# Kernel tuning notes

Measured on AMD Instinct MI355X. Metric: run time of the kernel, lower is better.

Reference implementation:

```python
import jax, jax.numpy as jnp
import numpy as np

B, T, D_IN, H, NUM_OUT = 64, 2048, 128, 512, 128


def _lstm_layer(x, W_ih, W_hh, b_ih, b_hh):
    # x: [B, T, D]; W_ih: [4H, D]; W_hh: [4H, H]; gate order i, f, g, o (PyTorch)
    Bsz = x.shape[0]
    Hh = W_hh.shape[1]
    # Precompute the input projection for all timesteps in one big GEMM: [B, T, 4H]
    xg = jnp.einsum('btd,gd->btg', x, W_ih) + b_ih + b_hh
    h0 = jnp.zeros((Bsz, Hh), x.dtype)
    c0 = jnp.zeros((Bsz, Hh), x.dtype)

    def step(carry, xg_t):
        h, c = carry
        gates = xg_t + h @ W_hh.T  # [B, 4H]
        i, f, g, o = jnp.split(gates, 4, axis=-1)
        i = jax.nn.sigmoid(i)
        f = jax.nn.sigmoid(f)
        g = jnp.tanh(g)
        o = jax.nn.sigmoid(o)
        c = f * c + i * g
        h = o * jnp.tanh(c)
        return (h, c), h

    (_, _), hs = jax.lax.scan(step, (h0, c0), jnp.swapaxes(xg, 0, 1))  # hs: [T, B, H]
    return jnp.swapaxes(hs, 0, 1)  # [B, T, H]


def setup_inputs() -> dict:
    key = jax.random.key(0)
    ks = jax.random.split(key, 7)

    def xavier(k, shape):
        fan_in, fan_out = shape[1], shape[0]
        lim = np.sqrt(6.0 / (fan_in + fan_out))
        return jax.random.uniform(k, shape, jnp.float32, -lim, lim)

    return {
        'x': jax.random.normal(ks[0], (B, T, D_IN), jnp.float32),
        'W_ih0': xavier(ks[1], (4 * H, D_IN)),
        'W_hh0': xavier(ks[2], (4 * H, H)),
        'b_ih0': jnp.zeros((4 * H,), jnp.float32),
        'b_hh0': jnp.zeros((4 * H,), jnp.float32),
        'W_ih1': xavier(ks[3], (4 * H, H)),
        'W_hh1': xavier(ks[4], (4 * H, H)),
        'b_ih1': jnp.zeros((4 * H,), jnp.float32),
        'b_hh1': jnp.zeros((4 * H,), jnp.float32),
        'fc_w': xavier(ks[5], (NUM_OUT, H)),
        'fc_b': jnp.zeros((NUM_OUT,), jnp.float32),
    }


def reference(x, W_ih0, W_hh0, b_ih0, b_hh0, W_ih1, W_hh1, b_ih1, b_hh1, fc_w, fc_b):
    out = _lstm_layer(x, W_ih0, W_hh0, b_ih0, b_hh0)
    out = _lstm_layer(out, W_ih1, W_hh1, b_ih1, b_hh1)
    # fc applied to last timestep only
    return out[:, -1, :] @ fc_w.T + fc_b
```

## Files before the change

kernel.cpp:

```cpp
#include <hip/hip_runtime.h>
#include <hip/hip_fp16.h>
#include <math.h>

#define BB    64
#define TT    2048
#define DIN   128
#define HH    512
#define NWG   256
#define NTHR  256
#define NUNITS 1152

typedef __attribute__((ext_vector_type(4))) unsigned int u32x4;
typedef __attribute__((ext_vector_type(8))) _Float16    f16x8;
typedef __attribute__((ext_vector_type(4))) float       f32x4;
typedef unsigned long long u64;

__device__ __forceinline__ float sigm(float v) { return 1.0f / (1.0f + expf(-v)); }

__device__ __forceinline__ u32x4 ld16m(const void* p) {
  u32x4 v;
  asm volatile("global_load_dwordx4 %0, %1, off sc0 sc1" : "=v"(v) : "v"(p) : "memory");
  return v;
}
__device__ __forceinline__ void st8m(void* p, u64 v) {
  __hip_atomic_store((u64*)p, v, __ATOMIC_RELAXED, __HIP_MEMORY_SCOPE_AGENT);
}
__device__ __forceinline__ u64 ld8m(const void* p) {
  return __hip_atomic_load((const u64*)p, __ATOMIC_RELAXED, __HIP_MEMORY_SCOPE_AGENT);
}

__global__ __launch_bounds__(64, 1) void prep_flush() {
  extern __shared__ char dummy[];
  if (threadIdx.x == 0) { __threadfence(); dummy[0] = 0; }
  __syncthreads();
}
__global__ void prep_zero(unsigned* w) {
  const int total = (4*BB*HH*2 + 8192) / 4;
  for (int i = blockIdx.x*blockDim.x + threadIdx.x; i < total; i += gridDim.x*blockDim.x)
    __hip_atomic_store(w + i, 0u, __ATOMIC_RELAXED, __HIP_MEMORY_SCOPE_AGENT);
}
__global__ void xcvt(const float* __restrict__ x, u64* __restrict__ xh) {
  const int N4 = BB*TT*DIN/4;
  const float4* x4 = reinterpret_cast<const float4*>(x);
  for (int i = blockIdx.x*blockDim.x + threadIdx.x; i < N4; i += gridDim.x*blockDim.x) {
    float4 v = x4[i];
    __half2 a = __floats2half2_rn(v.x, v.y);
    __half2 b = __floats2half2_rn(v.z, v.w);
    u64 u = ((u64)__builtin_bit_cast(unsigned, b) << 32) | (u64)__builtin_bit_cast(unsigned, a);
    __hip_atomic_store(&xh[i], u, __ATOMIC_RELAXED, __HIP_MEMORY_SCOPE_AGENT);
  }
}

__global__ __launch_bounds__(NTHR, 1) void lstm2_fb(
    const float* __restrict__ Wih0, const float* __restrict__ Whh0,
    const float* __restrict__ bih0, const float* __restrict__ bhh0,
    const float* __restrict__ Wih1, const float* __restrict__ Whh1,
    const float* __restrict__ bih1, const float* __restrict__ bhh1,
    const float* __restrict__ fcw,  const float* __restrict__ fcb,
    float* __restrict__ out, float* __restrict__ ws)
{
  extern __shared__ char smbase[];
  __half* hout = reinterpret_cast<__half*>(smbase + 18432);
  int*    dead = reinterpret_cast<int*>(smbase + 18944);

  const int tid  = threadIdx.x;
  const int wg   = blockIdx.x;
  const int lane = tid & 63;
  const int wv   = tid >> 6;

  const int grp  = wg >> 5;
  const int r    = wg & 31;
  const int bg8  = grp * 8;
  const int c0   = 16*r + 4*wv;

  __half* h0s = reinterpret_cast<__half*>(ws);
  __half* h1s = h0s + 2*BB*HH;
  unsigned* flg = reinterpret_cast<unsigned*>((char*)ws + 262144) + grp*32;
  const __half* xh = reinterpret_cast<const __half*>((char*)ws + 524288);

  const int rt   = lane & 15;
  const int gate = rt & 3;
  const int jc   = rt >> 2;
  const int kg   = lane >> 4;
  const int b15  = lane & 15;
  const int n0   = gate*HH + (c0 + jc);

  f16x8 af0[20];
#pragma unroll
  for (int m = 0; m < 20; ++m) {
    int k0 = 32*m + 8*kg;
    const float* srcp = (k0 < DIN) ? (Wih0 + (size_t)n0*DIN + k0)
                                   : (Whh0 + (size_t)n0*HH + (k0 - DIN));
    float4 a = *reinterpret_cast<const float4*>(srcp);
    float4 b = *reinterpret_cast<const float4*>(srcp + 4);
    f16x8 fr;
    fr[0]=(_Float16)a.x; fr[1]=(_Float16)a.y; fr[2]=(_Float16)a.z; fr[3]=(_Float16)a.w;
    fr[4]=(_Float16)b.x; fr[5]=(_Float16)b.y; fr[6]=(_Float16)b.z; fr[7]=(_Float16)b.w;
    af0[m] = fr;
  }
  f16x8 af1[32];
#pragma unroll
  for (int m = 0; m < 32; ++m) {
    int k0 = 32*m + 8*kg;
    const float* srcp = (k0 < HH) ? (Wih1 + (size_t)n0*HH + k0)
                                  : (Whh1 + (size_t)n0*HH + (k0 - HH));
    float4 a = *reinterpret_cast<const float4*>(srcp);
    float4 b = *reinterpret_cast<const float4*>(srcp + 4);
    f16x8 fr;
    fr[0]=(_Float16)a.x; fr[1]=(_Float16)a.y; fr[2]=(_Float16)a.z; fr[3]=(_Float16)a.w;
    fr[4]=(_Float16)b.x; fr[5]=(_Float16)b.y; fr[6]=(_Float16)b.z; fr[7]=(_Float16)b.w;
    af1[m] = fr;
  }

  const int cmy = c0 + kg;
  float bv0[4], bv1[4];
#pragma unroll
  for (int g = 0; g < 4; ++g) {
    bv0[g] = bih0[g*HH + cmy] + bhh0[g*HH + cmy];
    bv1[g] = bih1[g*HH + cmy] + bhh1[g*HH + cmy];
  }

  float cst0 = 0.f, cst1 = 0.f;
  const int beff = (b15 < 8) ? b15 : 7;
  const int bsw  = beff << 1;
  if (tid == 0) *dead = 0;
  __syncthreads();

  for (int st = 0; st <= TT; ++st) {
    const int tcur = (st < TT) ? st : (TT - 1);
    const __half* h0r = h0s + (size_t)(st & 1)*BB*HH;
    const __half* h1r = h1s + (size_t)(st & 1)*BB*HH;

    u32x4 stgL[5];
    int   physv[5];
#pragma unroll
    for (int ii = 0; ii < 5; ++ii) {
      int idx = tid + NTHR*ii;
      physv[ii] = -1;
      if (idx < NUNITS) {
        const __half* src; int phys;
        if (idx < 128)      { int b = idx>>4, u = idx&15;
          src = xh + (size_t)(bg8+b)*TT*DIN + (size_t)tcur*DIN + u*8;
          phys = b*16 + (u ^ ((b<<1)&15)); }
        else if (idx < 640) { int i2 = idx-128, b = i2>>6, u = i2&63;
          src = h0r + (size_t)(bg8+b)*HH + u*8;
          phys = 128 + b*64 + (u ^ (b<<1)); }
        else                { int i2 = idx-640, b = i2>>6, u = i2&63;
          src = h1r + (size_t)(bg8+b)*HH + u*8;
          phys = 640 + b*64 + (u ^ (b<<1)); }
        physv[ii] = phys;
        stgL[ii] = ld16m(src);
      }
    }
    asm volatile("s_waitcnt vmcnt(0)" ::: "memory");
    __builtin_amdgcn_sched_barrier(0);
#pragma unroll
    for (int ii = 0; ii < 5; ++ii)
      if (physv[ii] >= 0)
        *reinterpret_cast<u32x4*>(smbase + physv[ii]*16) = stgL[ii];
    __syncthreads();

    f32x4 a0a = {0.f,0.f,0.f,0.f}, a0b = a0a, a1a = a0a, a1b = a0a;
#pragma unroll
    for (int m = 0; m < 20; ++m) {
      int phys = (m < 4) ? (beff*16 + ((4*m + kg) ^ (bsw & 15)))
                         : (128 + beff*64 + ((4*(m-4) + kg) ^ bsw));
      f16x8 bf = *reinterpret_cast<const f16x8*>(smbase + phys*16);
      if (m & 1) a0b = __builtin_amdgcn_mfma_f32_16x16x32_f16(af0[m], bf, a0b, 0, 0, 0);
      else       a0a = __builtin_amdgcn_mfma_f32_16x16x32_f16(af0[m], bf, a0a, 0, 0, 0);
    }
#pragma unroll
    for (int m = 0; m < 32; ++m) {
      int phys = (m < 16) ? (128 + beff*64 + ((4*m + kg) ^ bsw))
                          : (640 + beff*64 + ((4*(m-16) + kg) ^ bsw));
      f16x8 bf = *reinterpret_cast<const f16x8*>(smbase + phys*16);
      if (m & 1) a1b = __builtin_amdgcn_mfma_f32_16x16x32_f16(af1[m], bf, a1b, 0, 0, 0);
      else       a1a = __builtin_amdgcn_mfma_f32_16x16x32_f16(af1[m], bf, a1a, 0, 0, 0);
    }
    f32x4 a0 = a0a + a0b;
    f32x4 a1 = a1a + a1b;

    if (st < TT) {
      float gi = sigm (a0[0] + bv0[0]);
      float gf = sigm (a0[1] + bv0[1]);
      float gg = tanhf(a0[2] + bv0[2]);
      float go = sigm (a0[3] + bv0[3]);
      cst0 = gf*cst0 + gi*gg;
      float hn = go * tanhf(cst0);
      if (b15 < 8) hout[(0*8 + b15)*16 + 4*wv + kg] = __float2half(hn);
    }
    if (st >= 1) {
      float gi = sigm (a1[0] + bv1[0]);
      float gf = sigm (a1[1] + bv1[1]);
      float gg = tanhf(a1[2] + bv1[2]);
      float go = sigm (a1[3] + bv1[3]);
      cst1 = gf*cst1 + gi*gg;
      float hn = go * tanhf(cst1);
      if (b15 < 8) hout[(1*8 + b15)*16 + 4*wv + kg] = __float2half(hn);
    }
    __syncthreads();

    if (tid < 64) {
      int layer = tid >> 5, q = tid & 31, b = q >> 2, part = q & 3;
      bool do_st = (layer == 0) ? (st < TT) : (st >= 1);
      if (do_st) {
        u64 v = *reinterpret_cast<u64*>(hout + (layer*8 + b)*16 + part*4);
        __half* base = (layer ? h1s : h0s) + (size_t)((st + 1) & 1)*BB*HH;
        st8m(base + (size_t)(bg8+b)*HH + 16*r + part*4, v);
      }
    }

    __syncthreads();
    if (wv == 0 && *dead == 0) {
      asm volatile("s_waitcnt vmcnt(0)" ::: "memory");
      if (lane == 0)
        __hip_atomic_store(flg + r, (unsigned)(st + 1),
                           __ATOMIC_RELAXED, __HIP_MEMORY_SCOPE_AGENT);
      long sp = 0;
      for (;;) {
        unsigned f = 0u;
        if (lane < 32)
          f = __hip_atomic_load(flg + lane, __ATOMIC_RELAXED, __HIP_MEMORY_SCOPE_AGENT);
        bool ok = (lane < 32) ? (f >= (unsigned)(st + 1)) : true;
        if (__all(ok)) break;
        __builtin_amdgcn_s_sleep(1);
        if (++sp > (1L << 22)) { if (lane == 0) *dead = 1; break; }
      }
      asm volatile("" ::: "memory");
    }
    __syncthreads();
  }

  {
    const __half* h1f = h1s + (size_t)BB*HH;
    int oi = tid >> 3, kp = tid & 7;
    int b  = oi >> 2, cc = oi & 3;
    int ocol = 4*r + cc;
    const u64* h8 = reinterpret_cast<const u64*>(h1f + (size_t)(bg8+b)*HH) + kp*16;
    const float* wrow = fcw + (size_t)ocol*HH + kp*64;
    float p = 0.f;
#pragma unroll
    for (int kk = 0; kk < 16; ++kk) {
      u64 v = ld8m(h8 + kk);
      __half2 hlo = __builtin_bit_cast(__half2, (unsigned)(v & 0xffffffffull));
      __half2 hhi = __builtin_bit_cast(__half2, (unsigned)(v >> 32));
      float2 flo = __half22float2(hlo), fhi = __half22float2(hhi);
      float4 w = *reinterpret_cast<const float4*>(wrow + kk*4);
      p += flo.x*w.x + flo.y*w.y + fhi.x*w.z + fhi.y*w.w;
    }
    p += __shfl_xor(p, 1);
    p += __shfl_xor(p, 2);
    p += __shfl_xor(p, 4);
    if (kp == 0) out[(size_t)(bg8+b)*128 + ocol] = p + fcb[ocol];
  }
}

__global__ void sentinel_fail(float* out, float v) { out[threadIdx.x] = v; }

extern "C" void kernel_launch(void* const* d_in, const int* in_sizes, int n_in,
                              void* d_out, int out_size, void* d_ws, size_t ws_size,
                              hipStream_t stream) {
  const float* x    = (const float*)d_in[0];
  const float* Wih0 = (const float*)d_in[1];
  const float* Whh0 = (const float*)d_in[2];
  const float* bih0 = (const float*)d_in[3];
  const float* bhh0 = (const float*)d_in[4];
  const float* Wih1 = (const float*)d_in[5];
  const float* Whh1 = (const float*)d_in[6];
  const float* bih1 = (const float*)d_in[7];
  const float* bhh1 = (const float*)d_in[8];
  const float* fcw  = (const float*)d_in[9];
  const float* fcb  = (const float*)d_in[10];
  float* out = (float*)d_out;
  float* ws  = (float*)d_ws;
  (void)in_sizes; (void)n_in; (void)out_size;

  const size_t need = 524288 + (size_t)BB*TT*DIN*2;
  if (ws_size < need) {
    sentinel_fail<<<1, 128, 0, stream>>>(out, 2.0e6f);
    return;
  }

  const int smem_bytes = 108*1024;
  hipFuncSetAttribute(reinterpret_cast<const void*>(&lstm2_fb),
                      hipFuncAttributeMaxDynamicSharedMemorySize, smem_bytes);
  hipFuncSetAttribute(reinterpret_cast<const void*>(&prep_flush),
                      hipFuncAttributeMaxDynamicSharedMemorySize, smem_bytes);

  (void)hipGetLastError();
  prep_flush<<<dim3(NWG), dim3(64), smem_bytes, stream>>>();
  xcvt<<<dim3(2048), dim3(NTHR), 0, stream>>>(
      x, reinterpret_cast<u64*>(reinterpret_cast<char*>(d_ws) + 524288));
  prep_zero<<<dim3(NWG), dim3(NTHR), 0, stream>>>((unsigned*)d_ws);
  lstm2_fb<<<dim3(NWG), dim3(NTHR), smem_bytes, stream>>>(
      Wih0, Whh0, bih0, bhh0, Wih1, Whh1, bih1, bhh1, fcw, fcb, out, ws);
  hipError_t e = hipGetLastError();
  if (e != hipSuccess) {
    sentinel_fail<<<1, 128, 0, stream>>>(out, 1.0e6f);
  }
}
```

Before: 8.455 ms.

## Split per-step grid barrier into two staggered flag phases per layer

Replaces the single end-of-step group barrier with two flag arrays. Layer-0 h is published and the layer-1 h buffer is read in a separate phase, and each workgroup polls only the flags it needs before loading. The layer-1 MFMA work on h0 now overlaps with waiting for other workgroups' h1 state. The intent is to shorten the serialized critical path of each timestep. It adds an extra __syncthreads and a second poll per step, and the double-buffer ordering becomes harder to verify.

```diff
diff --git a/kernel.cpp b/kernel.cpp
--- a/kernel.cpp
+++ b/kernel.cpp
@@ -8,7 +8,6 @@
 #define HH    512
 #define NWG   256
 #define NTHR  256
-#define NUNITS 1152
 
 typedef __attribute__((ext_vector_type(4))) unsigned int u32x4;
 typedef __attribute__((ext_vector_type(8))) _Float16    f16x8;
@@ -28,6 +27,20 @@
 __device__ __forceinline__ u64 ld8m(const void* p) {
   return __hip_atomic_load((const u64*)p, __ATOMIC_RELAXED, __HIP_MEMORY_SCOPE_AGENT);
 }
+__device__ __forceinline__ void fpoll(unsigned* flags, unsigned target, int lane, int* dead) {
+  if (*dead) return;
+  long sp = 0;
+  for (;;) {
+    unsigned f = 0u;
+    if (lane < 32)
+      f = __hip_atomic_load(flags + lane, __ATOMIC_RELAXED, __HIP_MEMORY_SCOPE_AGENT);
+    bool ok = (lane < 32) ? (f >= target) : true;
+    if (__all(ok)) break;
+    __builtin_amdgcn_s_sleep(1);
+    if (++sp > (1L << 22)) { if (lane == 0) *dead = 1; break; }
+  }
+  asm volatile("" ::: "memory");
+}
 
 __global__ __launch_bounds__(64, 1) void prep_flush() {
   extern __shared__ char dummy[];
@@ -35,7 +48,7 @@
   __syncthreads();
 }
 __global__ void prep_zero(unsigned* w) {
-  const int total = (4*BB*HH*2 + 8192) / 4;
+  const int total = (4*BB*HH*2 + 16384) / 4;
   for (int i = blockIdx.x*blockDim.x + threadIdx.x; i < total; i += gridDim.x*blockDim.x)
     __hip_atomic_store(w + i, 0u, __ATOMIC_RELAXED, __HIP_MEMORY_SCOPE_AGENT);
 }
@@ -51,7 +64,7 @@
   }
 }
 
-__global__ __launch_bounds__(NTHR, 1) void lstm2_fb(
+__global__ __launch_bounds__(NTHR, 1) void lstm2_sp(
     const float* __restrict__ Wih0, const float* __restrict__ Whh0,
     const float* __restrict__ bih0, const float* __restrict__ bhh0,
     const float* __restrict__ Wih1, const float* __restrict__ Whh1,
@@ -75,7 +88,8 @@
 
   __half* h0s = reinterpret_cast<__half*>(ws);
   __half* h1s = h0s + 2*BB*HH;
-  unsigned* flg = reinterpret_cast<unsigned*>((char*)ws + 262144) + grp*32;
+  unsigned* flgA = reinterpret_cast<unsigned*>((char*)ws + 262144) + grp*32;
+  unsigned* flgB = reinterpret_cast<unsigned*>((char*)ws + 266240) + grp*32;
   const __half* xh = reinterpret_cast<const __half*>((char*)ws + 524288);
 
   const int rt   = lane & 15;
@@ -131,33 +145,34 @@
     const __half* h0r = h0s + (size_t)(st & 1)*BB*HH;
     const __half* h1r = h1s + (size_t)(st & 1)*BB*HH;
 
-    u32x4 stgL[5];
-    int   physv[5];
-#pragma unroll
-    for (int ii = 0; ii < 5; ++ii) {
+    if (wv == 0) fpoll(flgA, (unsigned)st, lane, dead);
+    __syncthreads();
+
+    u32x4 stgA[3]; int phyA[3];
+#pragma unroll
+    for (int ii = 0; ii < 3; ++ii) {
       int idx = tid + NTHR*ii;
-      physv[ii] = -1;
-      if (idx < NUNITS) {
+      phyA[ii] = -1;
+      if (idx < 640) {
         const __half* src; int phys;
-        if (idx < 128)      { int b = idx>>4, u = idx&15;
+        if (idx < 128) { int b = idx>>4, u = idx&15;
           src = xh + (size_t)(bg8+b)*TT*DIN + (size_t)tcur*DIN + u*8;
           phys = b*16 + (u ^ ((b<<1)&15)); }
-        else if (idx < 640) { int i2 = idx-128, b = i2>>6, u = i2&63;
+        else           { int i2 = idx-128, b = i2>>6, u = i2&63;
           src = h0r + (size_t)(bg8+b)*HH + u*8;
           phys = 128 + b*64 + (u ^ (b<<1)); }
-        else                { int i2 = idx-640, b = i2>>6, u = i2&63;
-          src = h1r + (size_t)(bg8+b)*HH + u*8;
-          phys = 640 + b*64 + (u ^ (b<<1)); }
-        physv[ii] = phys;
-        stgL[ii] = ld16m(src);
+        phyA[ii] = phys;
+        stgA[ii] = ld16m(src);
       }
     }
     asm volatile("s_waitcnt vmcnt(0)" ::: "memory");
     __builtin_amdgcn_sched_barrier(0);
-#pragma unroll
-    for (int ii = 0; ii < 5; ++ii)
-      if (physv[ii] >= 0)
-        *reinterpret_cast<u32x4*>(smbase + physv[ii]*16) = stgL[ii];
+    if (tid == 0)
+      __hip_atomic_store(flgB + r, (unsigned)st, __ATOMIC_RELAXED, __HIP_MEMORY_SCOPE_AGENT);
+#pragma unroll
+    for (int ii = 0; ii < 3; ++ii)
+      if (phyA[ii] >= 0)
+        *reinterpret_cast<u32x4*>(smbase + phyA[ii]*16) = stgA[ii];
     __syncthreads();
 
     f32x4 a0a = {0.f,0.f,0.f,0.f}, a0b = a0a, a1a = a0a, a1b = a0a;
@@ -170,17 +185,15 @@
       else       a0a = __builtin_amdgcn_mfma_f32_16x16x32_f16(af0[m], bf, a0a, 0, 0, 0);
     }
 #pragma unroll
-    for (int m = 0; m < 32; ++m) {
-      int phys = (m < 16) ? (128 + beff*64 + ((4*m + kg) ^ bsw))
-                          : (640 + beff*64 + ((4*(m-16) + kg) ^ bsw));
+    for (int m = 0; m < 16; ++m) {
+      int phys = 128 + beff*64 + ((4*m + kg) ^ bsw);
       f16x8 bf = *reinterpret_cast<const f16x8*>(smbase + phys*16);
       if (m & 1) a1b = __builtin_amdgcn_mfma_f32_16x16x32_f16(af1[m], bf, a1b, 0, 0, 0);
       else       a1a = __builtin_amdgcn_mfma_f32_16x16x32_f16(af1[m], bf, a1a, 0, 0, 0);
     }
-    f32x4 a0 = a0a + a0b;
-    f32x4 a1 = a1a + a1b;
 
     if (st < TT) {
+      f32x4 a0 = a0a + a0b;
       float gi = sigm (a0[0] + bv0[0]);
       float gf = sigm (a0[1] + bv0[1]);
       float gg = tanhf(a0[2] + bv0[2]);
@@ -189,7 +202,46 @@
       float hn = go * tanhf(cst0);
       if (b15 < 8) hout[(0*8 + b15)*16 + 4*wv + kg] = __float2half(hn);
     }
+    __syncthreads();
+
+    if (tid < 32 && st < TT) {
+      int b = tid >> 2, part = tid & 3;
+      u64 v = *reinterpret_cast<u64*>(hout + (0*8 + b)*16 + part*4);
+      __half* base = h0s + (size_t)((st + 1) & 1)*BB*HH;
+      st8m(base + (size_t)(bg8+b)*HH + 16*r + part*4, v);
+    }
+    if (wv == 1) fpoll(flgB, (unsigned)st, lane, dead);
+    __syncthreads();
+
+    u32x4 stgB[2];
+#pragma unroll
+    for (int ii = 0; ii < 2; ++ii) {
+      int idx = tid + NTHR*ii;
+      int b = idx >> 6, u = idx & 63;
+      stgB[ii] = ld16m(h1r + (size_t)(bg8+b)*HH + u*8);
+    }
+    asm volatile("s_waitcnt vmcnt(0)" ::: "memory");
+    __builtin_amdgcn_sched_barrier(0);
+    if (tid == 0)
+      __hip_atomic_store(flgA + r, (unsigned)(st + 1), __ATOMIC_RELAXED, __HIP_MEMORY_SCOPE_AGENT);
+#pragma unroll
+    for (int ii = 0; ii < 2; ++ii) {
+      int idx = tid + NTHR*ii;
+      int b = idx >> 6, u = idx & 63;
+      *reinterpret_cast<u32x4*>(smbase + (640 + b*64 + (u ^ (b<<1)))*16) = stgB[ii];
+    }
+    __syncthreads();
+
+#pragma unroll
+    for (int m = 16; m < 32; ++m) {
+      int phys = 640 + beff*64 + ((4*(m-16) + kg) ^ bsw);
+      f16x8 bf = *reinterpret_cast<const f16x8*>(smbase + phys*16);
+      if (m & 1) a1b = __builtin_amdgcn_mfma_f32_16x16x32_f16(af1[m], bf, a1b, 0, 0, 0);
+      else       a1a = __builtin_amdgcn_mfma_f32_16x16x32_f16(af1[m], bf, a1a, 0, 0, 0);
+    }
+
     if (st >= 1) {
+      f32x4 a1 = a1a + a1b;
       float gi = sigm (a1[0] + bv1[0]);
       float gf = sigm (a1[1] + bv1[1]);
       float gg = tanhf(a1[2] + bv1[2]);
@@ -200,37 +252,19 @@
     }
     __syncthreads();
 
-    if (tid < 64) {
-      int layer = tid >> 5, q = tid & 31, b = q >> 2, part = q & 3;
-      bool do_st = (layer == 0) ? (st < TT) : (st >= 1);
-      if (do_st) {
-        u64 v = *reinterpret_cast<u64*>(hout + (layer*8 + b)*16 + part*4);
-        __half* base = (layer ? h1s : h0s) + (size_t)((st + 1) & 1)*BB*HH;
-        st8m(base + (size_t)(bg8+b)*HH + 16*r + part*4, v);
-      }
-    }
-
-    __syncthreads();
-    if (wv == 0 && *dead == 0) {
-      asm volatile("s_waitcnt vmcnt(0)" ::: "memory");
-      if (lane == 0)
-        __hip_atomic_store(flg + r, (unsigned)(st + 1),
-                           __ATOMIC_RELAXED, __HIP_MEMORY_SCOPE_AGENT);
-      long sp = 0;
-      for (;;) {
-        unsigned f = 0u;
-        if (lane < 32)
-          f = __hip_atomic_load(flg + lane, __ATOMIC_RELAXED, __HIP_MEMORY_SCOPE_AGENT);
-        bool ok = (lane < 32) ? (f >= (unsigned)(st + 1)) : true;
-        if (__all(ok)) break;
-        __builtin_amdgcn_s_sleep(1);
-        if (++sp > (1L << 22)) { if (lane == 0) *dead = 1; break; }
-      }
-      asm volatile("" ::: "memory");
-    }
-    __syncthreads();
-  }
-
+    if (tid < 32 && st >= 1) {
+      int b = tid >> 2, part = tid & 3;
+      u64 v = *reinterpret_cast<u64*>(hout + (1*8 + b)*16 + part*4);
+      __half* base = h1s + (size_t)((st + 1) & 1)*BB*HH;
+      st8m(base + (size_t)(bg8+b)*HH + 16*r + part*4, v);
+    }
+  }
+
+  asm volatile("s_waitcnt vmcnt(0)" ::: "memory");
+  if (tid == 0)
+    __hip_atomic_store(flgB + r, (unsigned)(TT + 1), __ATOMIC_RELAXED, __HIP_MEMORY_SCOPE_AGENT);
+  if (wv == 0) fpoll(flgB, (unsigned)(TT + 1), lane, dead);
+  __syncthreads();
   {
     const __half* h1f = h1s + (size_t)BB*HH;
     int oi = tid >> 3, kp = tid & 7;
@@ -282,7 +316,7 @@
   }
 
   const int smem_bytes = 108*1024;
-  hipFuncSetAttribute(reinterpret_cast<const void*>(&lstm2_fb),
+  hipFuncSetAttribute(reinterpret_cast<const void*>(&lstm2_sp),
                       hipFuncAttributeMaxDynamicSharedMemorySize, smem_bytes);
   hipFuncSetAttribute(reinterpret_cast<const void*>(&prep_flush),
                       hipFuncAttributeMaxDynamicSharedMemorySize, smem_bytes);
@@ -292,7 +326,7 @@
   xcvt<<<dim3(2048), dim3(NTHR), 0, stream>>>(
       x, reinterpret_cast<u64*>(reinterpret_cast<char*>(d_ws) + 524288));
   prep_zero<<<dim3(NWG), dim3(NTHR), 0, stream>>>((unsigned*)d_ws);
-  lstm2_fb<<<dim3(NWG), dim3(NTHR), smem_bytes, stream>>>(
+  lstm2_sp<<<dim3(NWG), dim3(NTHR), smem_bytes, stream>>>(
       Wih0, Whh0, bih0, bhh0, Wih1, Whh1, bih1, bhh1, fcw, fcb, out, ws);
   hipError_t e = hipGetLastError();
   if (e != hipSuccess) {
```

New measurement: 7.729 ms, median of 2. -8.6%, faster.
